# Kernel optimization log

Hardware: AMD Instinct MI355X
Metric: run time of the kernel (lower is better)

The kernel has to match this reference:

```python
import jax, jax.numpy as jnp
import numpy as np

TEMP = 1.0  # softmax temperature (self.temp)
S, B, V, E, H, R, ER = 256, 8, 32000, 300, 512, 46, 64


def setup_inputs() -> dict:
    key = jax.random.key(0)
    ks = jax.random.split(key, 12)
    w = lambda k, shape, s=0.02: jax.random.normal(k, shape, jnp.float32) * s
    return {
        "tokens": jax.random.randint(ks[0], (S, B), 0, V, dtype=jnp.int32),
        "relations": jax.random.randint(ks[1], (S, B), 0, R, dtype=jnp.int32),
        "hiddens": jax.random.normal(ks[2], (B, H), jnp.float32),
        "embed_weight": w(ks[3], (V, E), 0.1),
        "transfer_weight": w(ks[4], (V, E), 0.1),
        "rel_emb": w(ks[5], (R, ER), 0.1),
        "W_ih": w(ks[6], (4 * H, E + ER)),
        "W_hh": w(ks[7], (4 * H, H)),
        "b_ih": jnp.zeros((4 * H,), jnp.float32),
        "b_hh": jnp.zeros((4 * H,), jnp.float32),
        "W_out": w(ks[8], (V, H)),
        "b_out": jnp.zeros((V,), jnp.float32),
    }


def _lstm_cell(x, h, c, W_ih, W_hh, b_ih, b_hh):
    gates = x @ W_ih.T + b_ih + h @ W_hh.T + b_hh  # [B, 4H]
    i, f, g, o = jnp.split(gates, 4, axis=-1)
    c = jax.nn.sigmoid(f) * c + jax.nn.sigmoid(i) * jnp.tanh(g)
    h = jax.nn.sigmoid(o) * jnp.tanh(c)
    return h, c


def reference(tokens, relations, hiddens, embed_weight, transfer_weight,
              rel_emb, W_ih, W_hh, b_ih, b_hh, W_out, b_out):
    # teacher-forced word inputs: SOS (row 0) then ground-truth prev token
    words = embed_weight[tokens]                              # [S,B,E]
    sos = jnp.broadcast_to(embed_weight[0], (1, tokens.shape[1], embed_weight.shape[1]))
    word_in = jnp.concatenate([sos, words[:-1]], axis=0)      # [S,B,E]
    rel_in = rel_emb[relations]                               # [S,B,ER]
    x_seq = jnp.concatenate([rel_in, word_in], axis=-1)       # [S,B,ER+E]

    def step(carry, x):
        h, c = carry
        h, c = _lstm_cell(x, h, c, W_ih, W_hh, b_ih, b_hh)
        return (h, c), h

    # original sets (h0, c0) = (hidden, hidden)
    (_, _), hs = jax.lax.scan(step, (hiddens, hiddens), x_seq)  # hs: [S,B,H]

    logits = hs @ W_out.T + b_out                             # [S,B,V]
    probs = jax.nn.softmax(logits / TEMP, axis=-1)
    soft = jnp.einsum("sbv,ve->sbe", probs, transfer_weight)  # soft embedding (grad path)
    hard = transfer_weight[jnp.argmax(probs, axis=-1)]        # .data overwrite with argmax emb
    return soft + jax.lax.stop_gradient(hard - soft)          # straight-through
```

## Files before the change

### kernel.cpp

```cpp
#include <hip/hip_runtime.h>
#include <math.h>

#define S_LEN 256
#define B_SZ 8
#define V_SZ 32000
#define E_SZ 300
#define H_SZ 512
#define ER_SZ 64
#define XD 364
#define G4H 2048
#define NCHUNK 500
#define NCAND 64

#define F_XPRE 0
#define F_HS32 (F_XPRE + 2048*2048)
#define F_H32  (F_HS32 + 2048*512)
#define F_C32  (F_H32 + 2*4096)
#define F_PV1  (F_C32 + 4096)
#define F_PV2  (F_PV1 + 2048*500)
#define F_I1   (F_PV2 + 2048*500)
#define F_I2   (F_I1 + 2048*500)

__global__ __launch_bounds__(256) void k_init(const float* __restrict__ hiddens,
                                              float* __restrict__ wsf) {
    int gid = blockIdx.x * 256 + threadIdx.x;
    if (gid < B_SZ * H_SZ) {
        float v = hiddens[gid];
        wsf[F_H32 + gid] = v;
        wsf[F_C32 + gid] = v;
    }
}

__global__ __launch_bounds__(256) void k_xpre(const int* __restrict__ tokens,
                                              const int* __restrict__ relations,
                                              const float* __restrict__ embed,
                                              const float* __restrict__ rel_emb,
                                              const float* __restrict__ W_ih,
                                              const float* __restrict__ b_ih,
                                              float* __restrict__ wsf) {
    __shared__ float xs[32][68];
    __shared__ float wsh[128][68];
    const int tid = threadIdx.x;
    const int sc = blockIdx.x >> 4;
    const int uc = blockIdx.x & 15;
    const int u0 = uc * 128;
    const int row0 = sc * 32;
    const int mg = tid >> 5;
    const int ng = tid & 31;
    float acc[4][4];
#pragma unroll
    for (int i = 0; i < 4; ++i)
#pragma unroll
        for (int j = 0; j < 4; ++j) acc[i][j] = 0.0f;

    for (int kt = 0; kt < 6; ++kt) {
#pragma unroll
        for (int i = 0; i < 2; ++i) {
            int f = tid + 256 * i;
            int r = f >> 4, kk4 = f & 15;
            int rowg = row0 + r;
            int s = rowg >> 3, b = rowg & 7;
            float4 v = make_float4(0.f, 0.f, 0.f, 0.f);
            if (kt == 0) {
                int rid = relations[s * B_SZ + b];
                v = *(const float4*)(rel_emb + (size_t)rid * ER_SZ + kk4 * 4);
            } else {
                int col = (kt - 1) * 64 + kk4 * 4;
                if (col < E_SZ) {
                    int tok = (s == 0) ? 0 : tokens[(s - 1) * B_SZ + b];
                    v = *(const float4*)(embed + (size_t)tok * E_SZ + col);
                }
            }
            *(float4*)(&xs[r][kk4 * 4]) = v;
        }
#pragma unroll
        for (int i = 0; i < 8; ++i) {
            int f = tid + 256 * i;
            int u = f >> 4, kk4 = f & 15;
            int k = kt * 64 + kk4 * 4;
            float4 v = make_float4(0.f, 0.f, 0.f, 0.f);
            if (k < XD) v = *(const float4*)(W_ih + (size_t)(u0 + u) * XD + k);
            *(float4*)(&wsh[u][kk4 * 4]) = v;
        }
        __syncthreads();
#pragma unroll
        for (int kk4 = 0; kk4 < 16; ++kk4) {
            float4 bf[4];
#pragma unroll
            for (int j = 0; j < 4; ++j) bf[j] = *(const float4*)(&wsh[ng + 32 * j][kk4 * 4]);
#pragma unroll
            for (int i = 0; i < 4; ++i) {
                float4 af = *(const float4*)(&xs[mg + 8 * i][kk4 * 4]);
#pragma unroll
                for (int j = 0; j < 4; ++j) {
                    acc[i][j] = fmaf(af.x, bf[j].x, acc[i][j]);
                    acc[i][j] = fmaf(af.y, bf[j].y, acc[i][j]);
                    acc[i][j] = fmaf(af.z, bf[j].z, acc[i][j]);
                    acc[i][j] = fmaf(af.w, bf[j].w, acc[i][j]);
                }
            }
        }
        __syncthreads();
    }
#pragma unroll
    for (int j = 0; j < 4; ++j) {
        int gu = u0 + ng + 32 * j;
        float bi = b_ih[gu];
#pragma unroll
        for (int i = 0; i < 4; ++i) {
            int rowg = row0 + mg + 8 * i;
            wsf[F_XPRE + (size_t)rowg * G4H + gu] = __fadd_rn(acc[i][j], bi);
        }
    }
}

__global__ __launch_bounds__(256) void k_step(const float* __restrict__ W_hh,
                                              const float* __restrict__ b_hh,
                                              float* __restrict__ wsf, int t) {
    __shared__ float hsh[8 * 520];
    __shared__ float gsh[4][8][8];
    const int tid = threadIdx.x;
    const int bid = blockIdx.x;
    const float* hsrc = wsf + F_H32 + (t & 1) * (B_SZ * H_SZ);
#pragma unroll
    for (int n = 0; n < 16; ++n) {
        int idx = n * 256 + tid;
        hsh[(idx >> 9) * 520 + (idx & 511)] = hsrc[idx];
    }
    __syncthreads();
    const int g = tid >> 6;
    const int ul = (tid >> 3) & 7;
    const int b = tid & 7;
    const int unit = bid * 8 + ul;
    const int grow = g * H_SZ + unit;
    const float* wrow = W_hh + (size_t)grow * H_SZ;
    const float* hrow = hsh + b * 520;
    float acc = 0.0f;
    for (int k = 0; k < H_SZ; ++k) acc = fmaf(wrow[k], hrow[k], acc);
    float xp = wsf[F_XPRE + (size_t)t * (B_SZ * G4H) + b * G4H + grow];
    float gate = __fadd_rn(__fadd_rn(xp, acc), b_hh[grow]);
    gsh[g][ul][b] = (g == 2) ? (float)tanh((double)gate)
                             : (float)(1.0 / (1.0 + exp(-(double)gate)));
    __syncthreads();
    if (tid < 64) {
        int ul2 = tid >> 3, b2 = tid & 7;
        float si = gsh[0][ul2][b2];
        float sf = gsh[1][ul2][b2];
        float tg = gsh[2][ul2][b2];
        float so = gsh[3][ul2][b2];
        int hidx = b2 * H_SZ + bid * 8 + ul2;
        float cp = wsf[F_C32 + hidx];
        float cn = __fadd_rn(__fmul_rn(sf, cp), __fmul_rn(si, tg));
        wsf[F_C32 + hidx] = cn;
        float hn = __fmul_rn(so, (float)tanh((double)cn));
        wsf[F_H32 + (size_t)((t + 1) & 1) * (B_SZ * H_SZ) + hidx] = hn;
        wsf[F_HS32 + (size_t)t * (B_SZ * H_SZ) + hidx] = hn;
    }
}

__device__ __forceinline__ void merge2(float& v1, int& i1, float& v2, int& i2,
                                       float ov1, int oi1, float ov2, int oi2) {
    if (ov1 > v1 || (ov1 == v1 && oi1 < i1)) {
        float nv2; int ni2;
        if (v1 > ov2 || (v1 == ov2 && i1 < oi2)) { nv2 = v1; ni2 = i1; }
        else { nv2 = ov2; ni2 = oi2; }
        v1 = ov1; i1 = oi1; v2 = nv2; i2 = ni2;
    } else {
        if (ov1 > v2 || (ov1 == v2 && oi1 < i2)) { v2 = ov1; i2 = oi1; }
    }
}

__global__ __launch_bounds__(256) void k_logits(const float* __restrict__ W_out,
                                                const float* __restrict__ b_out,
                                                float* __restrict__ wsf) {
    __shared__ float hssh[128][68];
    __shared__ float wsh2[64][68];
    const int tid = threadIdx.x;
    const int mt = blockIdx.x & 15;
    const int vc = blockIdx.x >> 4;
    const int m0 = mt * 128, v0 = vc * 64;
    const int mg = tid >> 4;
    const int ng = tid & 15;
    const float* hs32 = wsf + F_HS32;
    float acc[8][4];
#pragma unroll
    for (int i = 0; i < 8; ++i)
#pragma unroll
        for (int j = 0; j < 4; ++j) acc[i][j] = 0.0f;

    for (int kt = 0; kt < 8; ++kt) {
#pragma unroll
        for (int i = 0; i < 8; ++i) {
            int f = tid + 256 * i;
            int r = f >> 4, kk4 = f & 15;
            *(float4*)(&hssh[r][kk4 * 4]) =
                *(const float4*)(hs32 + (size_t)(m0 + r) * H_SZ + kt * 64 + kk4 * 4);
        }
#pragma unroll
        for (int i = 0; i < 4; ++i) {
            int f = tid + 256 * i;
            int v = f >> 4, kk4 = f & 15;
            *(float4*)(&wsh2[v][kk4 * 4]) =
                *(const float4*)(W_out + (size_t)(v0 + v) * H_SZ + kt * 64 + kk4 * 4);
        }
        __syncthreads();
#pragma unroll
        for (int kk4 = 0; kk4 < 16; ++kk4) {
            float4 bf[4];
#pragma unroll
            for (int j = 0; j < 4; ++j) bf[j] = *(const float4*)(&wsh2[ng + 16 * j][kk4 * 4]);
#pragma unroll
            for (int i = 0; i < 8; ++i) {
                float4 af = *(const float4*)(&hssh[mg + 16 * i][kk4 * 4]);
#pragma unroll
                for (int j = 0; j < 4; ++j) {
                    acc[i][j] = fmaf(af.x, bf[j].x, acc[i][j]);
                    acc[i][j] = fmaf(af.y, bf[j].y, acc[i][j]);
                    acc[i][j] = fmaf(af.z, bf[j].z, acc[i][j]);
                    acc[i][j] = fmaf(af.w, bf[j].w, acc[i][j]);
                }
            }
        }
        __syncthreads();
    }
    float bo[4];
#pragma unroll
    for (int j = 0; j < 4; ++j) bo[j] = b_out[v0 + ng + 16 * j];
#pragma unroll
    for (int i = 0; i < 8; ++i) {
        float v1 = acc[i][0] + bo[0];
        int i1 = v0 + ng;
        float v2 = -1e30f; int i2 = 0x7fffffff;
#pragma unroll
        for (int j = 1; j < 4; ++j) {
            float v = acc[i][j] + bo[j];
            int ix = v0 + ng + 16 * j;
            if (v > v1 || (v == v1 && ix < i1)) { v2 = v1; i2 = i1; v1 = v; i1 = ix; }
            else if (v > v2 || (v == v2 && ix < i2)) { v2 = v; i2 = ix; }
        }
#pragma unroll
        for (int off = 8; off >= 1; off >>= 1) {
            float ov1 = __shfl_down(v1, off, 16);
            int oi1 = __shfl_down(i1, off, 16);
            float ov2 = __shfl_down(v2, off, 16);
            int oi2 = __shfl_down(i2, off, 16);
            merge2(v1, i1, v2, i2, ov1, oi1, ov2, oi2);
        }
        if (ng == 0) {
            int rowg = m0 + mg + 16 * i;
            wsf[F_PV1 + (size_t)rowg * NCHUNK + vc] = v1;
            wsf[F_PV2 + (size_t)rowg * NCHUNK + vc] = v2;
            ((int*)wsf)[F_I1 + (size_t)rowg * NCHUNK + vc] = i1;
            ((int*)wsf)[F_I2 + (size_t)rowg * NCHUNK + vc] = i2;
        }
    }
}

__global__ __launch_bounds__(256) void k_out(const float* __restrict__ transfer,
                                             const float* __restrict__ W_out,
                                             const float* __restrict__ b_out,
                                             const float* __restrict__ wsf,
                                             float* __restrict__ out) {
    __shared__ int cand[4][NCAND];
    __shared__ int cnt[4];
    __shared__ int chosen[4];
    const float* pv1 = wsf + F_PV1;
    const float* pv2 = wsf + F_PV2;
    const int* pi1 = (const int*)wsf + F_I1;
    const int* pi2 = (const int*)wsf + F_I2;
    const float* hs32 = wsf + F_HS32;
    const int tid = threadIdx.x;
    const int wv = tid >> 6, lane = tid & 63;
    const int row = blockIdx.x * 4 + wv;
    if (tid < 4) cnt[tid] = 0;
    __syncthreads();
    float m = -1e30f;
    for (int c = lane; c < NCHUNK; c += 64) m = fmaxf(m, pv1[(size_t)row * NCHUNK + c]);
#pragma unroll
    for (int off = 32; off >= 1; off >>= 1) m = fmaxf(m, __shfl_xor(m, off, 64));
    float thr = m - 1e-3f;
    for (int c = lane; c < NCHUNK; c += 64) {
        float a = pv1[(size_t)row * NCHUNK + c];
        if (a >= thr) {
            int p = atomicAdd(&cnt[wv], 1);
            if (p < NCAND) cand[wv][p] = pi1[(size_t)row * NCHUNK + c];
        }
        float bq = pv2[(size_t)row * NCHUNK + c];
        if (bq >= thr) {
            int p = atomicAdd(&cnt[wv], 1);
            if (p < NCAND) cand[wv][p] = pi2[(size_t)row * NCHUNK + c];
        }
    }
    __syncthreads();
    int nc = cnt[wv];
    if (nc > NCAND) nc = NCAND;
    bool active = (lane < nc);
    int v = active ? cand[wv][lane] : 0x7fffffff;
    float l32 = -1e30f;
    if (active && v >= 0 && v < V_SZ) {
        const float* wr = W_out + (size_t)v * H_SZ;
        const float* hr = hs32 + (size_t)row * H_SZ;
        float s = 0.0f;
        for (int k = 0; k < H_SZ; ++k) s = fmaf(wr[k], hr[k], s);
        l32 = __fadd_rn(s, b_out[v]);
    }
    float m32 = l32;
#pragma unroll
    for (int off = 32; off >= 1; off >>= 1) m32 = fmaxf(m32, __shfl_xor(m32, off, 64));
    float p = active ? expf(l32 - m32) : -1.0f;
#pragma unroll
    for (int off = 32; off >= 1; off >>= 1) {
        float op = __shfl_xor(p, off, 64);
        int ov = __shfl_xor(v, off, 64);
        if (op > p || (op == p && ov < v)) { p = op; v = ov; }
    }
    if (lane == 0) {
        if (v < 0 || v >= V_SZ) v = 0;
        chosen[wv] = v;
    }
    __syncthreads();
    for (int f = tid; f < 300; f += 256) {
        int r = f / 75, e4 = f - r * 75;
        float4 val = *(const float4*)(transfer + (size_t)chosen[r] * E_SZ + e4 * 4);
        *(float4*)(out + (size_t)(blockIdx.x * 4 + r) * E_SZ + e4 * 4) = val;
    }
}

extern "C" void kernel_launch(void* const* d_in, const int* in_sizes, int n_in,
                              void* d_out, int out_size, void* d_ws, size_t ws_size,
                              hipStream_t stream) {
    const int* tokens = (const int*)d_in[0];
    const int* relations = (const int*)d_in[1];
    const float* hiddens = (const float*)d_in[2];
    const float* embed = (const float*)d_in[3];
    const float* transfer = (const float*)d_in[4];
    const float* rel_emb = (const float*)d_in[5];
    const float* W_ih = (const float*)d_in[6];
    const float* W_hh = (const float*)d_in[7];
    const float* b_ih = (const float*)d_in[8];
    const float* b_hh = (const float*)d_in[9];
    const float* W_out = (const float*)d_in[10];
    const float* b_out = (const float*)d_in[11];
    float* wsf = (float*)d_ws;
    float* out = (float*)d_out;

    hipLaunchKernelGGL(k_init, dim3(16), dim3(256), 0, stream, hiddens, wsf);
    hipLaunchKernelGGL(k_xpre, dim3(1024), dim3(256), 0, stream,
                       tokens, relations, embed, rel_emb, W_ih, b_ih, wsf);
    for (int t = 0; t < S_LEN; ++t)
        hipLaunchKernelGGL(k_step, dim3(64), dim3(256), 0, stream, W_hh, b_hh, wsf, t);
    hipLaunchKernelGGL(k_logits, dim3(16 * NCHUNK), dim3(256), 0, stream, W_out, b_out, wsf);
    hipLaunchKernelGGL(k_out, dim3(512), dim3(256), 0, stream,
                       transfer, W_out, b_out, wsf, out);
}
```

Before: 3.427 ms.

## Replace per-step LSTM launches with a persistent kernel using a global flag barrier

The 256 per-timestep kernel launches become a single persistent kernel of 64 blocks. The blocks synchronise each timestep through per-block progress flags in workspace memory, using atomic stores and spin-waiting. The cell state stays in registers, and the W_hh dot product is vectorised with float4 loads. This removes launch overhead and the inter-kernel gaps on the serial recurrence, but it depends on all 64 blocks being co-resident and adds spin-wait and memory-fence costs at every step.

Result: slower. 5.685 ms (+65.9%).

```diff
diff --git a/kernel.cpp b/kernel.cpp
--- a/kernel.cpp
+++ b/kernel.cpp
@@ -11,6 +11,7 @@
 #define G4H 2048
 #define NCHUNK 500
 #define NCAND 64
+#define NB_LSTM 64
 
 #define F_XPRE 0
 #define F_HS32 (F_XPRE + 2048*2048)
@@ -20,15 +21,15 @@
 #define F_PV2  (F_PV1 + 2048*500)
 #define F_I1   (F_PV2 + 2048*500)
 #define F_I2   (F_I1 + 2048*500)
+#define F_FLAGS (F_I2 + 2048*500)
 
 __global__ __launch_bounds__(256) void k_init(const float* __restrict__ hiddens,
                                               float* __restrict__ wsf) {
     int gid = blockIdx.x * 256 + threadIdx.x;
     if (gid < B_SZ * H_SZ) {
-        float v = hiddens[gid];
-        wsf[F_H32 + gid] = v;
-        wsf[F_C32 + gid] = v;
-    }
+        wsf[F_H32 + gid] = hiddens[gid];
+    }
+    if (gid < NB_LSTM) ((int*)wsf)[F_FLAGS + gid] = 0;
 }
 
 __global__ __launch_bounds__(256) void k_xpre(const int* __restrict__ tokens,
@@ -114,47 +115,82 @@
     }
 }
 
-__global__ __launch_bounds__(256) void k_step(const float* __restrict__ W_hh,
-                                              const float* __restrict__ b_hh,
-                                              float* __restrict__ wsf, int t) {
-    __shared__ float hsh[8 * 520];
+__global__ __launch_bounds__(256, 1) void k_lstm(const float* __restrict__ W_hh,
+                                                 const float* __restrict__ b_hh,
+                                                 const float* __restrict__ hiddens,
+                                                 float* __restrict__ wsf) {
+    __shared__ float hsh[8 * 516];
     __shared__ float gsh[4][8][8];
     const int tid = threadIdx.x;
     const int bid = blockIdx.x;
-    const float* hsrc = wsf + F_H32 + (t & 1) * (B_SZ * H_SZ);
-#pragma unroll
-    for (int n = 0; n < 16; ++n) {
-        int idx = n * 256 + tid;
-        hsh[(idx >> 9) * 520 + (idx & 511)] = hsrc[idx];
-    }
-    __syncthreads();
     const int g = tid >> 6;
     const int ul = (tid >> 3) & 7;
     const int b = tid & 7;
     const int unit = bid * 8 + ul;
     const int grow = g * H_SZ + unit;
-    const float* wrow = W_hh + (size_t)grow * H_SZ;
-    const float* hrow = hsh + b * 520;
-    float acc = 0.0f;
-    for (int k = 0; k < H_SZ; ++k) acc = fmaf(wrow[k], hrow[k], acc);
-    float xp = wsf[F_XPRE + (size_t)t * (B_SZ * G4H) + b * G4H + grow];
-    float gate = __fadd_rn(__fadd_rn(xp, acc), b_hh[grow]);
-    gsh[g][ul][b] = (g == 2) ? (float)tanh((double)gate)
-                             : (float)(1.0 / (1.0 + exp(-(double)gate)));
-    __syncthreads();
+    const float4* w4 = (const float4*)(W_hh + (size_t)grow * H_SZ);
+    const float bhh = b_hh[grow];
+    int* flags = (int*)wsf + F_FLAGS;
+
+    float creg = 0.0f;
     if (tid < 64) {
         int ul2 = tid >> 3, b2 = tid & 7;
-        float si = gsh[0][ul2][b2];
-        float sf = gsh[1][ul2][b2];
-        float tg = gsh[2][ul2][b2];
-        float so = gsh[3][ul2][b2];
-        int hidx = b2 * H_SZ + bid * 8 + ul2;
-        float cp = wsf[F_C32 + hidx];
-        float cn = __fadd_rn(__fmul_rn(sf, cp), __fmul_rn(si, tg));
-        wsf[F_C32 + hidx] = cn;
-        float hn = __fmul_rn(so, (float)tanh((double)cn));
-        wsf[F_H32 + (size_t)((t + 1) & 1) * (B_SZ * H_SZ) + hidx] = hn;
-        wsf[F_HS32 + (size_t)t * (B_SZ * H_SZ) + hidx] = hn;
+        creg = hiddens[b2 * H_SZ + bid * 8 + ul2];
+    }
+
+    for (int t = 0; t < S_LEN; ++t) {
+        const float* hsrc = wsf + F_H32 + (t & 1) * (B_SZ * H_SZ);
+#pragma unroll
+        for (int n = 0; n < 16; ++n) {
+            int idx = n * 256 + tid;
+            float v = __hip_atomic_load(hsrc + idx, __ATOMIC_RELAXED, __HIP_MEMORY_SCOPE_AGENT);
+            hsh[(idx >> 9) * 516 + (idx & 511)] = v;
+        }
+        __syncthreads();
+        float xp = wsf[F_XPRE + (size_t)t * (B_SZ * G4H) + b * G4H + grow];
+        const float4* h4 = (const float4*)(hsh + b * 516);
+        float acc = 0.0f;
+#pragma unroll 8
+        for (int i = 0; i < 128; ++i) {
+            float4 wv = w4[i];
+            float4 hv = h4[i];
+            acc = fmaf(wv.x, hv.x, acc);
+            acc = fmaf(wv.y, hv.y, acc);
+            acc = fmaf(wv.z, hv.z, acc);
+            acc = fmaf(wv.w, hv.w, acc);
+        }
+        float gate = __fadd_rn(__fadd_rn(xp, acc), bhh);
+        gsh[g][ul][b] = (g == 2) ? (float)tanh((double)gate)
+                                 : (float)(1.0 / (1.0 + exp(-(double)gate)));
+        __syncthreads();
+        if (tid < 64) {
+            int ul2 = tid >> 3, b2 = tid & 7;
+            float si = gsh[0][ul2][b2];
+            float sf = gsh[1][ul2][b2];
+            float tg = gsh[2][ul2][b2];
+            float so = gsh[3][ul2][b2];
+            float cn = __fadd_rn(__fmul_rn(sf, creg), __fmul_rn(si, tg));
+            creg = cn;
+            float hn = __fmul_rn(so, (float)tanh((double)cn));
+            int hidx = b2 * H_SZ + bid * 8 + ul2;
+            __hip_atomic_store(wsf + F_H32 + ((t + 1) & 1) * (B_SZ * H_SZ) + hidx, hn,
+                               __ATOMIC_RELAXED, __HIP_MEMORY_SCOPE_AGENT);
+            wsf[F_HS32 + (size_t)t * (B_SZ * H_SZ) + hidx] = hn;
+        }
+        __syncthreads();
+        if (tid == 0) {
+            __threadfence();
+            __hip_atomic_store(flags + bid, t + 1, __ATOMIC_RELEASE, __HIP_MEMORY_SCOPE_AGENT);
+        }
+        int done;
+        do {
+            int pred = 1;
+            if (tid < NB_LSTM)
+                pred = (__hip_atomic_load(flags + tid, __ATOMIC_RELAXED,
+                                          __HIP_MEMORY_SCOPE_AGENT) >= (t + 1));
+            done = __syncthreads_count(pred);
+        } while (done < 256);
+        __threadfence();
     }
 }
 
@@ -347,8 +383,8 @@
     hipLaunchKernelGGL(k_init, dim3(16), dim3(256), 0, stream, hiddens, wsf);
     hipLaunchKernelGGL(k_xpre, dim3(1024), dim3(256), 0, stream,
                        tokens, relations, embed, rel_emb, W_ih, b_ih, wsf);
-    for (int t = 0; t < S_LEN; ++t)
-        hipLaunchKernelGGL(k_step, dim3(64), dim3(256), 0, stream, W_hh, b_hh, wsf, t);
+    hipLaunchKernelGGL(k_lstm, dim3(NB_LSTM), dim3(256), 0, stream,
+                       W_hh, b_hh, hiddens, wsf);
     hipLaunchKernelGGL(k_logits, dim3(16 * NCHUNK), dim3(256), 0, stream, W_out, b_out, wsf);
     hipLaunchKernelGGL(k_out, dim3(512), dim3(256), 0, stream,
                        transfer, W_out, b_out, wsf, out);
```
